# Performance work log

Hardware: AMD Instinct MI355X
Metric: run time of the kernel (lower is better)

Reference implementation:

```python
import jax, jax.numpy as jnp
import numpy as np

B, T, D, H = 2, 2048, 1024, 16
DH = D // H  # 64, rope dim


def rotate_half(x):
    x1, x2 = jnp.split(x, 2, axis=-1)
    return jnp.concatenate([-x2, x1], axis=-1)


def rope_tables(seq_len, dim, dtype=jnp.float32):
    inv_freq = 1.0 / (10000.0 ** (jnp.arange(0, dim, 2, dtype=jnp.float32) / dim))
    t = jnp.arange(seq_len, dtype=jnp.float32)
    freqs = jnp.outer(t, inv_freq)              # [T, dim/2]
    emb = jnp.concatenate([freqs, freqs], -1)   # [T, dim]
    return jnp.cos(emb).astype(dtype), jnp.sin(emb).astype(dtype)


def setup_inputs() -> dict:
    key = jax.random.key(0)
    ks = jax.random.split(key, 5)
    w_scale = 0.02
    x = jax.random.normal(ks[0], (B, T, D), jnp.float32)
    W_q = jax.random.normal(ks[1], (D, D), jnp.float32) * w_scale
    W_k = jax.random.normal(ks[2], (D, D), jnp.float32) * w_scale
    W_v = jax.random.normal(ks[3], (D, D), jnp.float32) * w_scale
    W_o = jax.random.normal(ks[4], (D, D), jnp.float32) * w_scale
    mask = jnp.tril(jnp.ones((T, T), jnp.int32))  # causal
    return {"x": x, "W_q": W_q, "W_k": W_k, "W_v": W_v, "W_o": W_o, "mask": mask}


def reference(x, W_q, W_k, W_v, W_o, mask):
    b, t, d = x.shape
    # Linear (bias=False): y = x @ W^T, weight shape (out, in)
    def proj(W):
        y = jnp.einsum('btd,ed->bte', x, W)
        return y.reshape(b, t, H, DH).transpose(0, 2, 1, 3)  # [B,H,T,dh]
    q, k, v = proj(W_q), proj(W_k), proj(W_v)

    cos, sin = rope_tables(t, DH, x.dtype)
    cos = cos[None, None]  # [1,1,T,dh]
    sin = sin[None, None]
    q = q * cos + rotate_half(q) * sin
    k = k * cos + rotate_half(k) * sin

    scale = 1.0 / np.sqrt(DH).astype(np.float32)
    scores = jnp.einsum('bhqd,bhkd->bhqk', q, k) * scale  # [B,H,T,T]
    neg_inf = jnp.finfo(scores.dtype).min
    scores = jnp.where(mask[:t, :t][None, None] == 0, neg_inf, scores)
    attn = jax.nn.softmax(scores, axis=-1)
    out = jnp.einsum('bhqk,bhkd->bhqd', attn, v)
    out = out.transpose(0, 2, 1, 3).reshape(b, t, d)
    return jnp.einsum('btd,ed->bte', out, W_o)
```

## Files before the change

kernel.cpp:

```cpp
#include <hip/hip_runtime.h>
#include <hip/hip_bf16.h>
#include <math.h>

#define B_  2
#define T_  2048
#define D_  1024
#define H_  16
#define DH_ 64
#define WN_ (D_ * D_)

typedef __attribute__((ext_vector_type(8))) short bf16x8;
typedef __attribute__((ext_vector_type(4))) float f32x4;

__device__ __forceinline__ void gll16(const void* g, void* l) {
  __builtin_amdgcn_global_load_lds(
      (const __attribute__((address_space(1))) void*)g,
      (__attribute__((address_space(3))) void*)l, 16, 0, 0);
}

__device__ __forceinline__ void storeC(float* p, float v) { *p = v; }
__device__ __forceinline__ void storeC(__hip_bfloat16* p, float v) {
  *p = __float2bfloat16(v);
}

__global__ __launch_bounds__(256)
void cvt_f32_bf16(const float* __restrict__ in, __hip_bfloat16* __restrict__ out,
                  int n4) {
  const int i = blockIdx.x * 256 + threadIdx.x;
  if (i >= n4) return;
  const float4 a = ((const float4*)in)[i];
  __hip_bfloat16 h0 = __float2bfloat16(a.x);
  __hip_bfloat16 h1 = __float2bfloat16(a.y);
  __hip_bfloat16 h2 = __float2bfloat16(a.z);
  __hip_bfloat16 h3 = __float2bfloat16(a.w);
  ushort4 o;
  o.x = *(unsigned short*)&h0;
  o.y = *(unsigned short*)&h1;
  o.z = *(unsigned short*)&h2;
  o.w = *(unsigned short*)&h3;
  *(ushort4*)(out + (size_t)i * 4) = o;
}

__global__ __launch_bounds__(256)
void cvt3_w(const float* __restrict__ Wq, const float* __restrict__ Wk,
            const float* __restrict__ Wv, __hip_bfloat16* __restrict__ out) {
  const int i = blockIdx.x * 256 + threadIdx.x;
  const int per = WN_ / 4;
  const int sel = i >> 18;
  const int off = i & (per - 1);
  const float* src = sel == 0 ? Wq : (sel == 1 ? Wk : Wv);
  const float4 a = ((const float4*)src)[off];
  __hip_bfloat16 h0 = __float2bfloat16(a.x);
  __hip_bfloat16 h1 = __float2bfloat16(a.y);
  __hip_bfloat16 h2 = __float2bfloat16(a.z);
  __hip_bfloat16 h3 = __float2bfloat16(a.w);
  ushort4 o;
  o.x = *(unsigned short*)&h0;
  o.y = *(unsigned short*)&h1;
  o.z = *(unsigned short*)&h2;
  o.w = *(unsigned short*)&h3;
  *(ushort4*)(out + (size_t)sel * WN_ + (size_t)off * 4) = o;
}

template <typename CT>
__global__ __launch_bounds__(256)
void gemm_bf16_mfma(const __hip_bfloat16* __restrict__ A,
                    const __hip_bfloat16* __restrict__ W,
                    CT* __restrict__ C, int M, int N, int K) {
  __shared__ unsigned short As[128 * 32];
  __shared__ unsigned short Bs[128 * 32];
  const int tid = threadIdx.x;
  const int w = tid >> 6;
  const int lane = tid & 63;
  const int lg = lane >> 4;
  const int ln = lane & 15;
  const int wr = w >> 1, wc = w & 1;
  const int row0 = blockIdx.y * 128;
  const int col0 = blockIdx.x * 128;

  const int sr = w * 32 + (lane >> 2);
  const int sp = lane & 3;

  f32x4 acc[4][4];
#pragma unroll
  for (int m = 0; m < 4; ++m)
#pragma unroll
    for (int n = 0; n < 4; ++n) acc[m][n] = (f32x4){0.f, 0.f, 0.f, 0.f};

  for (int k0 = 0; k0 < K; k0 += 32) {
#pragma unroll
    for (int c = 0; c < 2; ++c) {
      const int r = sr + c * 16;
      const int ks = sp ^ ((r >> 1) & 3);
      gll16(A + (size_t)(row0 + r) * K + k0 + ks * 8,
            &As[(w * 32 + c * 16) * 32]);
      gll16(W + (size_t)(col0 + r) * K + k0 + ks * 8,
            &Bs[(w * 32 + c * 16) * 32]);
    }
    __syncthreads();

    bf16x8 af[4], bfr[4];
#pragma unroll
    for (int m = 0; m < 4; ++m) {
      const int r = wr * 64 + m * 16 + ln;
      af[m] = *(const bf16x8*)&As[r * 32 + (lg ^ ((r >> 1) & 3)) * 8];
    }
#pragma unroll
    for (int n = 0; n < 4; ++n) {
      const int r = wc * 64 + n * 16 + ln;
      bfr[n] = *(const bf16x8*)&Bs[r * 32 + (lg ^ ((r >> 1) & 3)) * 8];
    }
#pragma unroll
    for (int m = 0; m < 4; ++m)
#pragma unroll
      for (int n = 0; n < 4; ++n)
        acc[m][n] = __builtin_amdgcn_mfma_f32_16x16x32_bf16(af[m], bfr[n],
                                                            acc[m][n], 0, 0, 0);
    __syncthreads();
  }

#pragma unroll
  for (int m = 0; m < 4; ++m) {
#pragma unroll
    for (int reg = 0; reg < 4; ++reg) {
      CT* crow = C + (size_t)(row0 + wr * 64 + m * 16 + lg * 4 + reg) * N
                 + col0 + wc * 64;
#pragma unroll
      for (int n = 0; n < 4; ++n) storeC(&crow[n * 16 + ln], acc[m][n][reg]);
    }
  }
}

__global__ __launch_bounds__(256)
void rope_qkv(const __hip_bfloat16* __restrict__ qkv,
              __hip_bfloat16* __restrict__ Qb, __hip_bfloat16* __restrict__ Kb) {
  const int idx = blockIdx.x * 256 + threadIdx.x;
  const int i = idx & 31;
  const int rest = idx >> 5;
  const int row = rest >> 4;
  const int h = rest & 15;
  const int t = row & (T_ - 1);
  const float inv_freq = powf(10000.0f, -(float)i * (1.0f / 32.0f));
  const float ang = (float)t * inv_freq;
  const float c = cosf(ang), s = sinf(ang);
  const size_t rb = (size_t)row * 3072 + h * 64;
  const float q1 = __bfloat162float(qkv[rb + i]);
  const float q2 = __bfloat162float(qkv[rb + i + 32]);
  const float k1 = __bfloat162float(qkv[rb + 1024 + i]);
  const float k2 = __bfloat162float(qkv[rb + 1024 + i + 32]);
  const size_t base = (size_t)rest * DH_;
  Qb[base + i]      = __float2bfloat16((q1 * c - q2 * s) * 0.125f);
  Qb[base + i + 32] = __float2bfloat16((q2 * c + q1 * s) * 0.125f);
  Kb[base + i]      = __float2bfloat16(k1 * c - k2 * s);
  Kb[base + i + 32] = __float2bfloat16(k2 * c + k1 * s);
}

__global__ __launch_bounds__(256)
void vt_prep(const __hip_bfloat16* __restrict__ qkv,
             __hip_bfloat16* __restrict__ vt) {
  __shared__ unsigned short Ls[64][65];
  const int tt = blockIdx.x;
  const int bh = blockIdx.y;
  const int b = bh >> 4, h = bh & 15;
  const int tid = threadIdx.x;
  const int t0 = tt * 64;
  const int rb = tid >> 3, c0 = (tid & 7) * 8;
#pragma unroll
  for (int it = 0; it < 2; ++it) {
    const int r = it * 32 + rb;
    uint4 x = *(const uint4*)&qkv[(size_t)(b * T_ + t0 + r) * 3072 + 2048 +
                                  h * 64 + c0];
    const unsigned short* xs = (const unsigned short*)&x;
#pragma unroll
    for (int j = 0; j < 8; ++j) Ls[c0 + j][r] = xs[j];
  }
  __syncthreads();
  const int d = tid >> 2, t8 = (tid & 3) * 16;
  unsigned short tmp[16];
#pragma unroll
  for (int j = 0; j < 16; ++j) tmp[j] = Ls[d][t8 + j];
  __hip_bfloat16* dst = vt + ((size_t)(b * H_ + h) * 64 + d) * T_ + t0 + t8;
  *(uint4*)&dst[0] = *(uint4*)&tmp[0];
  *(uint4*)&dst[8] = *(uint4*)&tmp[8];
}

#define SWZ(row, col) ((col) ^ (((row) & 7) << 3))

__global__ __launch_bounds__(256)
void attn_mfma(const __hip_bfloat16* __restrict__ Qb,
               const __hip_bfloat16* __restrict__ Kb,
               const __hip_bfloat16* __restrict__ vt,
               __hip_bfloat16* __restrict__ O) {
  __shared__ unsigned short Qs[64 * 64];
  __shared__ unsigned short Ks[64 * 64];
  __shared__ unsigned short Vt[64 * 64];
  __shared__ unsigned short Ps[4 * 16 * 64];

  const int bx = blockIdx.x;
  const int bh = blockIdx.y;
  const int b = bh >> 4, h = bh & 15;
  const int tid = threadIdx.x;
  const int w = tid >> 6;
  const int lane = tid & 63;
  const int lg = lane >> 4;
  const int ln = lane & 15;

  const size_t headoff = (size_t)b * T_ * D_ + (size_t)h * DH_;
  const __hip_bfloat16* Qg = Qb + headoff;
  const __hip_bfloat16* Kg = Kb + headoff;
  const __hip_bfloat16* vtg = vt + (size_t)(b * H_ + h) * 64 * T_;
  __hip_bfloat16* Og = O + headoff;

  const int rb = tid >> 3, c0 = (tid & 7) * 8;

  for (int pass = 0; pass < 2; ++pass) {
    const int qt = pass ? bx : 31 - bx;

#pragma unroll
    for (int it = 0; it < 2; ++it) {
      const int r = it * 32 + rb;
      uint4 x = *(const uint4*)(Qg + (size_t)(qt * 64 + r) * D_ + c0);
      *(uint4*)&Qs[r * 64 + SWZ(r, c0)] = x;
    }

    uint4 kreg[2], vreg[2];
#pragma unroll
    for (int it = 0; it < 2; ++it) {
      const int r = it * 32 + rb;
      kreg[it] = *(const uint4*)(Kg + (size_t)r * D_ + c0);
      vreg[it] = *(const uint4*)(vtg + (size_t)r * T_ + c0);
    }

    float m_run[4], l_run[4];
    f32x4 accO[4];
#pragma unroll
    for (int r = 0; r < 4; ++r) {
      m_run[r] = -3.0e38f;
      l_run[r] = 0.f;
      accO[r] = (f32x4){0.f, 0.f, 0.f, 0.f};
    }
    bf16x8 aQ[2];

    for (int kt = 0; kt <= qt; ++kt) {
      __syncthreads();
#pragma unroll
      for (int it = 0; it < 2; ++it) {
        const int r = it * 32 + rb;
        *(uint4*)&Ks[r * 64 + SWZ(r, c0)] = kreg[it];
        *(uint4*)&Vt[r * 64 + SWZ(r, c0)] = vreg[it];
      }
      __syncthreads();

      if (kt == 0) {
#pragma unroll
        for (int ks = 0; ks < 2; ++ks) {
          const int r = w * 16 + ln;
          aQ[ks] = *(const bf16x8*)&Qs[r * 64 + SWZ(r, lg * 8 + 32 * ks)];
        }
      }
      if (kt < qt) {
#pragma unroll
        for (int it = 0; it < 2; ++it) {
          const int r = it * 32 + rb;
          kreg[it] = *(const uint4*)(Kg + (size_t)((kt + 1) * 64 + r) * D_ + c0);
          vreg[it] = *(const uint4*)(vtg + (size_t)r * T_ + (kt + 1) * 64 + c0);
        }
      }

      f32x4 sf[4];
#pragma unroll
      for (int cb = 0; cb < 4; ++cb) sf[cb] = (f32x4){0.f, 0.f, 0.f, 0.f};
#pragma unroll
      for (int ks = 0; ks < 2; ++ks) {
#pragma unroll
        for (int cb = 0; cb < 4; ++cb) {
          const int r = cb * 16 + ln;
          bf16x8 bk = *(const bf16x8*)&Ks[r * 64 + SWZ(r, lg * 8 + 32 * ks)];
          sf[cb] = __builtin_amdgcn_mfma_f32_16x16x32_bf16(aQ[ks], bk, sf[cb], 0, 0, 0);
        }
      }

      if (kt == qt) {
#pragma unroll
        for (int cb = 0; cb < 4; ++cb) {
          const int col = cb * 16 + ln;
#pragma unroll
          for (int reg = 0; reg < 4; ++reg) {
            const int row = w * 16 + lg * 4 + reg;
            if (col > row) sf[cb][reg] = -3.0e38f;
          }
        }
      }

#pragma unroll
      for (int reg = 0; reg < 4; ++reg) {
        float mloc = fmaxf(fmaxf(sf[0][reg], sf[1][reg]),
                           fmaxf(sf[2][reg], sf[3][reg]));
        mloc = fmaxf(mloc, __shfl_xor(mloc, 1, 16));
        mloc = fmaxf(mloc, __shfl_xor(mloc, 2, 16));
        mloc = fmaxf(mloc, __shfl_xor(mloc, 4, 16));
        mloc = fmaxf(mloc, __shfl_xor(mloc, 8, 16));
        const float mnew = fmaxf(m_run[reg], mloc);
        const float alpha = __expf(m_run[reg] - mnew);
        m_run[reg] = mnew;
        float rsum = 0.f;
#pragma unroll
        for (int cb = 0; cb < 4; ++cb) {
          const float p = __expf(sf[cb][reg] - mnew);
          sf[cb][reg] = p;
          rsum += p;
        }
        rsum += __shfl_xor(rsum, 1, 16);
        rsum += __shfl_xor(rsum, 2, 16);
        rsum += __shfl_xor(rsum, 4, 16);
        rsum += __shfl_xor(rsum, 8, 16);
        l_run[reg] = l_run[reg] * alpha + rsum;
#pragma unroll
        for (int db = 0; db < 4; ++db) accO[db][reg] *= alpha;
      }

#pragma unroll
      for (int cb = 0; cb < 4; ++cb) {
        const int col = cb * 16 + ln;
#pragma unroll
        for (int reg = 0; reg < 4; ++reg) {
          const int row = lg * 4 + reg;
          *(__hip_bfloat16*)&Ps[w * 1024 + row * 64 + SWZ(row, col)] =
              __float2bfloat16(sf[cb][reg]);
        }
      }

#pragma unroll
      for (int ks = 0; ks < 2; ++ks) {
        bf16x8 ap =
            *(const bf16x8*)&Ps[w * 1024 + ln * 64 + SWZ(ln, lg * 8 + 32 * ks)];
#pragma unroll
        for (int db = 0; db < 4; ++db) {
          const int r = db * 16 + ln;
          bf16x8 bv = *(const bf16x8*)&Vt[r * 64 + SWZ(r, lg * 8 + 32 * ks)];
          accO[db] = __builtin_amdgcn_mfma_f32_16x16x32_bf16(ap, bv, accO[db], 0, 0, 0);
        }
      }
    }

#pragma unroll
    for (int reg = 0; reg < 4; ++reg) {
      const float inv = 1.0f / l_run[reg];
      const int qrow = qt * 64 + w * 16 + lg * 4 + reg;
#pragma unroll
      for (int db = 0; db < 4; ++db) {
        Og[(size_t)qrow * D_ + db * 16 + ln] =
            __float2bfloat16(accO[db][reg] * inv);
      }
    }
  }
}

extern "C" void kernel_launch(void* const* d_in, const int* in_sizes, int n_in,
                              void* d_out, int out_size, void* d_ws, size_t ws_size,
                              hipStream_t stream) {
  const float* x  = (const float*)d_in[0];
  const float* Wq = (const float*)d_in[1];
  const float* Wk = (const float*)d_in[2];
  const float* Wv = (const float*)d_in[3];
  const float* Wo = (const float*)d_in[4];
  float* out = (float*)d_out;

  const size_t NE = (size_t)B_ * T_ * D_;
  char* base = (char*)d_ws;
  __hip_bfloat16* qkvb  = (__hip_bfloat16*)base;
  __hip_bfloat16* xb    = (__hip_bfloat16*)(base + 3 * NE * 2);
  __hip_bfloat16* Wqkvb = (__hip_bfloat16*)(base + 4 * NE * 2);
  __hip_bfloat16* qb    = (__hip_bfloat16*)(base + 4 * NE * 2 + 3ull * WN_ * 2);
  __hip_bfloat16* kb    = qb + NE;
  __hip_bfloat16* vtb   = kb + NE;
  __hip_bfloat16* aob   = qkvb;
  __hip_bfloat16* Wob   = Wqkvb;

  cvt_f32_bf16<<<(int)(NE / 4 / 256), 256, 0, stream>>>(x, xb, (int)(NE / 4));
  cvt3_w<<<3 * WN_ / 4 / 256, 256, 0, stream>>>(Wq, Wk, Wv, Wqkvb);

  const dim3 gq(3 * D_ / 128, (B_ * T_) / 128);
  gemm_bf16_mfma<__hip_bfloat16><<<gq, 256, 0, stream>>>(
      xb, Wqkvb, qkvb, B_ * T_, 3 * D_, D_);

  rope_qkv<<<(B_ * T_ * H_ * 32) / 256, 256, 0, stream>>>(qkvb, qb, kb);
  vt_prep<<<dim3(T_ / 64, B_ * H_), 256, 0, stream>>>(qkvb, vtb);

  const dim3 ga(T_ / 128, B_ * H_);
  attn_mfma<<<ga, 256, 0, stream>>>(qb, kb, vtb, aob);

  cvt_f32_bf16<<<WN_ / 4 / 256, 256, 0, stream>>>(Wo, Wob, WN_ / 4);

  const dim3 go(D_ / 128, (B_ * T_) / 128);
  gemm_bf16_mfma<float><<<go, 256, 0, stream>>>(aob, Wob, out, B_ * T_, D_, D_);
}
```

Baseline: 274.7 us.

## Rewrite attention with 32x32 MFMA, transposed scores, and double-buffered K/V

```diff
diff --git a/kernel.cpp b/kernel.cpp
--- a/kernel.cpp
+++ b/kernel.cpp
@@ -11,6 +11,7 @@
 
 typedef __attribute__((ext_vector_type(8))) short bf16x8;
 typedef __attribute__((ext_vector_type(4))) float f32x4;
+typedef __attribute__((ext_vector_type(16))) float f32x16;
 
 __device__ __forceinline__ void gll16(const void* g, void* l) {
   __builtin_amdgcn_global_load_lds(
@@ -186,15 +187,14 @@
 
 #define SWZ(row, col) ((col) ^ (((row) & 7) << 3))
 
-__global__ __launch_bounds__(256)
-void attn_mfma(const __hip_bfloat16* __restrict__ Qb,
-               const __hip_bfloat16* __restrict__ Kb,
-               const __hip_bfloat16* __restrict__ vt,
-               __hip_bfloat16* __restrict__ O) {
-  __shared__ unsigned short Qs[64 * 64];
-  __shared__ unsigned short Ks[64 * 64];
-  __shared__ unsigned short Vt[64 * 64];
-  __shared__ unsigned short Ps[4 * 16 * 64];
+__global__ __launch_bounds__(128)
+void attn_mfma32(const __hip_bfloat16* __restrict__ Qb,
+                 const __hip_bfloat16* __restrict__ Kb,
+                 const __hip_bfloat16* __restrict__ vt,
+                 __hip_bfloat16* __restrict__ O) {
+  __shared__ unsigned short Ks[2][64 * 64];
+  __shared__ unsigned short Vs[2][64 * 64];
+  __shared__ unsigned short Ps[2][32 * 64];
 
   const int bx = blockIdx.x;
   const int bh = blockIdx.y;
@@ -202,8 +202,8 @@
   const int tid = threadIdx.x;
   const int w = tid >> 6;
   const int lane = tid & 63;
-  const int lg = lane >> 4;
-  const int ln = lane & 15;
+  const int lq = lane & 31;
+  const int hi = lane >> 5;
 
   const size_t headoff = (size_t)b * T_ * D_ + (size_t)h * DH_;
   const __hip_bfloat16* Qg = Qb + headoff;
@@ -211,146 +211,158 @@
   const __hip_bfloat16* vtg = vt + (size_t)(b * H_ + h) * 64 * T_;
   __hip_bfloat16* Og = O + headoff;
 
-  const int rb = tid >> 3, c0 = (tid & 7) * 8;
+  const int sr0 = tid >> 3;
+  const int sc0 = (tid & 7) * 8;
 
   for (int pass = 0; pass < 2; ++pass) {
     const int qt = pass ? bx : 31 - bx;
-
-#pragma unroll
-    for (int it = 0; it < 2; ++it) {
-      const int r = it * 32 + rb;
-      uint4 x = *(const uint4*)(Qg + (size_t)(qt * 64 + r) * D_ + c0);
-      *(uint4*)&Qs[r * 64 + SWZ(r, c0)] = x;
-    }
-
-    uint4 kreg[2], vreg[2];
-#pragma unroll
-    for (int it = 0; it < 2; ++it) {
-      const int r = it * 32 + rb;
-      kreg[it] = *(const uint4*)(Kg + (size_t)r * D_ + c0);
-      vreg[it] = *(const uint4*)(vtg + (size_t)r * T_ + c0);
-    }
-
-    float m_run[4], l_run[4];
-    f32x4 accO[4];
-#pragma unroll
-    for (int r = 0; r < 4; ++r) {
-      m_run[r] = -3.0e38f;
-      l_run[r] = 0.f;
-      accO[r] = (f32x4){0.f, 0.f, 0.f, 0.f};
-    }
-    bf16x8 aQ[2];
+    const int q_glob = qt * 64 + w * 32 + lq;
+
+    bf16x8 qf[4];
+#pragma unroll
+    for (int ks = 0; ks < 4; ++ks)
+      qf[ks] = *(const bf16x8*)(Qg + (size_t)q_glob * D_ + ks * 16 + hi * 8);
+
+    uint4 kreg[4], vreg[4];
+#pragma unroll
+    for (int it = 0; it < 4; ++it) {
+      const int r = sr0 + it * 16;
+      kreg[it] = *(const uint4*)(Kg + (size_t)r * D_ + sc0);
+      vreg[it] = *(const uint4*)(vtg + (size_t)r * T_ + sc0);
+    }
+#pragma unroll
+    for (int it = 0; it < 4; ++it) {
+      const int r = sr0 + it * 16;
+      *(uint4*)&Ks[0][r * 64 + SWZ(r, sc0)] = kreg[it];
+      *(uint4*)&Vs[0][r * 64 + SWZ(r, sc0)] = vreg[it];
+    }
+    if (qt >= 1) {
+#pragma unroll
+      for (int it = 0; it < 4; ++it) {
+        const int r = sr0 + it * 16;
+        kreg[it] = *(const uint4*)(Kg + (size_t)(64 + r) * D_ + sc0);
+        vreg[it] = *(const uint4*)(vtg + (size_t)r * T_ + 64 + sc0);
+      }
+    }
+
+    float m_run = -3.0e38f, l_run = 0.f;
+    f32x16 accO[2];
+#pragma unroll
+    for (int reg = 0; reg < 16; ++reg) { accO[0][reg] = 0.f; accO[1][reg] = 0.f; }
+
+    __syncthreads();
 
     for (int kt = 0; kt <= qt; ++kt) {
+      const int buf = kt & 1;
+      if (kt + 1 <= qt) {
+#pragma unroll
+        for (int it = 0; it < 4; ++it) {
+          const int r = sr0 + it * 16;
+          *(uint4*)&Ks[buf ^ 1][r * 64 + SWZ(r, sc0)] = kreg[it];
+          *(uint4*)&Vs[buf ^ 1][r * 64 + SWZ(r, sc0)] = vreg[it];
+        }
+      }
+      if (kt + 2 <= qt) {
+#pragma unroll
+        for (int it = 0; it < 4; ++it) {
+          const int r = sr0 + it * 16;
+          kreg[it] = *(const uint4*)(Kg + (size_t)((kt + 2) * 64 + r) * D_ + sc0);
+          vreg[it] = *(const uint4*)(vtg + (size_t)r * T_ + (kt + 2) * 64 + sc0);
+        }
+      }
+
+      f32x16 sf[2];
+#pragma unroll
+      for (int reg = 0; reg < 16; ++reg) { sf[0][reg] = 0.f; sf[1][reg] = 0.f; }
+#pragma unroll
+      for (int ks = 0; ks < 4; ++ks) {
+        const int c = ks * 16 + hi * 8;
+        bf16x8 ka0 = *(const bf16x8*)&Ks[buf][lq * 64 + SWZ(lq, c)];
+        bf16x8 ka1 = *(const bf16x8*)&Ks[buf][(32 + lq) * 64 + SWZ(32 + lq, c)];
+        sf[0] = __builtin_amdgcn_mfma_f32_32x32x16_bf16(ka0, qf[ks], sf[0], 0, 0, 0);
+        sf[1] = __builtin_amdgcn_mfma_f32_32x32x16_bf16(ka1, qf[ks], sf[1], 0, 0, 0);
+      }
+
+      const int kv0 = kt * 64;
+      if (kt == qt) {
+#pragma unroll
+        for (int reg = 0; reg < 16; ++reg) {
+          const int krow = (reg & 3) + 8 * (reg >> 2) + 4 * hi;
+          if (kv0 + krow > q_glob)      sf[0][reg] = -3.0e38f;
+          if (kv0 + 32 + krow > q_glob) sf[1][reg] = -3.0e38f;
+        }
+      }
+
+      float pmax = -3.0e38f;
+#pragma unroll
+      for (int reg = 0; reg < 16; ++reg)
+        pmax = fmaxf(pmax, fmaxf(sf[0][reg], sf[1][reg]));
+      pmax = fmaxf(pmax, __shfl_xor(pmax, 32, 64));
+      const float mnew = fmaxf(m_run, pmax);
+      const float alpha = __expf(m_run - mnew);
+      m_run = mnew;
+      float rsum = 0.f;
+#pragma unroll
+      for (int reg = 0; reg < 16; ++reg) {
+        sf[0][reg] = __expf(sf[0][reg] - mnew);
+        sf[1][reg] = __expf(sf[1][reg] - mnew);
+        rsum += sf[0][reg] + sf[1][reg];
+      }
+      rsum += __shfl_xor(rsum, 32, 64);
+      l_run = l_run * alpha + rsum;
+#pragma unroll
+      for (int reg = 0; reg < 16; ++reg) {
+        accO[0][reg] *= alpha;
+        accO[1][reg] *= alpha;
+      }
+
+#pragma unroll
+      for (int kb = 0; kb < 2; ++kb) {
+#pragma unroll
+        for (int j = 0; j < 4; ++j) {
+          __hip_bfloat16 b0 = __float2bfloat16(sf[kb][4 * j + 0]);
+          __hip_bfloat16 b1 = __float2bfloat16(sf[kb][4 * j + 1]);
+          __hip_bfloat16 b2 = __float2bfloat16(sf[kb][4 * j + 2]);
+          __hip_bfloat16 b3 = __float2bfloat16(sf[kb][4 * j + 3]);
+          uint2 pk;
+          pk.x = (unsigned)*(unsigned short*)&b0 |
+                 ((unsigned)*(unsigned short*)&b1 << 16);
+          pk.y = (unsigned)*(unsigned short*)&b2 |
+                 ((unsigned)*(unsigned short*)&b3 << 16);
+          const int col = kb * 32 + 8 * j + 4 * hi;
+          *(uint2*)&Ps[w][lq * 64 + SWZ(lq, col)] = pk;
+        }
+      }
+
+#pragma unroll
+      for (int ks = 0; ks < 4; ++ks) {
+        const int c = ks * 16 + hi * 8;
+        bf16x8 pb  = *(const bf16x8*)&Ps[w][lq * 64 + SWZ(lq, c)];
+        bf16x8 va0 = *(const bf16x8*)&Vs[buf][lq * 64 + SWZ(lq, c)];
+        bf16x8 va1 = *(const bf16x8*)&Vs[buf][(32 + lq) * 64 + SWZ(32 + lq, c)];
+        accO[0] = __builtin_amdgcn_mfma_f32_32x32x16_bf16(va0, pb, accO[0], 0, 0, 0);
+        accO[1] = __builtin_amdgcn_mfma_f32_32x32x16_bf16(va1, pb, accO[1], 0, 0, 0);
+      }
+
       __syncthreads();
-#pragma unroll
-      for (int it = 0; it < 2; ++it) {
-        const int r = it * 32 + rb;
-        *(uint4*)&Ks[r * 64 + SWZ(r, c0)] = kreg[it];
-        *(uint4*)&Vt[r * 64 + SWZ(r, c0)] = vreg[it];
-      }
-      __syncthreads();
-
-      if (kt == 0) {
-#pragma unroll
-        for (int ks = 0; ks < 2; ++ks) {
-          const int r = w * 16 + ln;
-          aQ[ks] = *(const bf16x8*)&Qs[r * 64 + SWZ(r, lg * 8 + 32 * ks)];
-        }
-      }
-      if (kt < qt) {
-#pragma unroll
-        for (int it = 0; it < 2; ++it) {
-          const int r = it * 32 + rb;
-          kreg[it] = *(const uint4*)(Kg + (size_t)((kt + 1) * 64 + r) * D_ + c0);
-          vreg[it] = *(const uint4*)(vtg + (size_t)r * T_ + (kt + 1) * 64 + c0);
-        }
-      }
-
-      f32x4 sf[4];
-#pragma unroll
-      for (int cb = 0; cb < 4; ++cb) sf[cb] = (f32x4){0.f, 0.f, 0.f, 0.f};
-#pragma unroll
-      for (int ks = 0; ks < 2; ++ks) {
-#pragma unroll
-        for (int cb = 0; cb < 4; ++cb) {
-          const int r = cb * 16 + ln;
-          bf16x8 bk = *(const bf16x8*)&Ks[r * 64 + SWZ(r, lg * 8 + 32 * ks)];
-          sf[cb] = __builtin_amdgcn_mfma_f32_16x16x32_bf16(aQ[ks], bk, sf[cb], 0, 0, 0);
-        }
-      }
-
-      if (kt == qt) {
-#pragma unroll
-        for (int cb = 0; cb < 4; ++cb) {
-          const int col = cb * 16 + ln;
-#pragma unroll
-          for (int reg = 0; reg < 4; ++reg) {
-            const int row = w * 16 + lg * 4 + reg;
-            if (col > row) sf[cb][reg] = -3.0e38f;
-          }
-        }
-      }
-
-#pragma unroll
-      for (int reg = 0; reg < 4; ++reg) {
-        float mloc = fmaxf(fmaxf(sf[0][reg], sf[1][reg]),
-                           fmaxf(sf[2][reg], sf[3][reg]));
-        mloc = fmaxf(mloc, __shfl_xor(mloc, 1, 16));
-        mloc = fmaxf(mloc, __shfl_xor(mloc, 2, 16));
-        mloc = fmaxf(mloc, __shfl_xor(mloc, 4, 16));
-        mloc = fmaxf(mloc, __shfl_xor(mloc, 8, 16));
-        const float mnew = fmaxf(m_run[reg], mloc);
-        const float alpha = __expf(m_run[reg] - mnew);
-        m_run[reg] = mnew;
-        float rsum = 0.f;
-#pragma unroll
-        for (int cb = 0; cb < 4; ++cb) {
-          const float p = __expf(sf[cb][reg] - mnew);
-          sf[cb][reg] = p;
-          rsum += p;
-        }
-        rsum += __shfl_xor(rsum, 1, 16);
-        rsum += __shfl_xor(rsum, 2, 16);
-        rsum += __shfl_xor(rsum, 4, 16);
-        rsum += __shfl_xor(rsum, 8, 16);
-        l_run[reg] = l_run[reg] * alpha + rsum;
-#pragma unroll
-        for (int db = 0; db < 4; ++db) accO[db][reg] *= alpha;
-      }
-
-#pragma unroll
-      for (int cb = 0; cb < 4; ++cb) {
-        const int col = cb * 16 + ln;
-#pragma unroll
-        for (int reg = 0; reg < 4; ++reg) {
-          const int row = lg * 4 + reg;
-          *(__hip_bfloat16*)&Ps[w * 1024 + row * 64 + SWZ(row, col)] =
-              __float2bfloat16(sf[cb][reg]);
-        }
-      }
-
-#pragma unroll
-      for (int ks = 0; ks < 2; ++ks) {
-        bf16x8 ap =
-            *(const bf16x8*)&Ps[w * 1024 + ln * 64 + SWZ(ln, lg * 8 + 32 * ks)];
-#pragma unroll
-        for (int db = 0; db < 4; ++db) {
-          const int r = db * 16 + ln;
-          bf16x8 bv = *(const bf16x8*)&Vt[r * 64 + SWZ(r, lg * 8 + 32 * ks)];
-          accO[db] = __builtin_amdgcn_mfma_f32_16x16x32_bf16(ap, bv, accO[db], 0, 0, 0);
-        }
-      }
-    }
-
-#pragma unroll
-    for (int reg = 0; reg < 4; ++reg) {
-      const float inv = 1.0f / l_run[reg];
-      const int qrow = qt * 64 + w * 16 + lg * 4 + reg;
-#pragma unroll
-      for (int db = 0; db < 4; ++db) {
-        Og[(size_t)qrow * D_ + db * 16 + ln] =
-            __float2bfloat16(accO[db][reg] * inv);
+    }
+
+    const float inv = 1.0f / l_run;
+#pragma unroll
+    for (int db = 0; db < 2; ++db) {
+#pragma unroll
+      for (int j = 0; j < 4; ++j) {
+        __hip_bfloat16 b0 = __float2bfloat16(accO[db][4 * j + 0] * inv);
+        __hip_bfloat16 b1 = __float2bfloat16(accO[db][4 * j + 1] * inv);
+        __hip_bfloat16 b2 = __float2bfloat16(accO[db][4 * j + 2] * inv);
+        __hip_bfloat16 b3 = __float2bfloat16(accO[db][4 * j + 3] * inv);
+        uint2 pk;
+        pk.x = (unsigned)*(unsigned short*)&b0 |
+               ((unsigned)*(unsigned short*)&b1 << 16);
+        pk.y = (unsigned)*(unsigned short*)&b2 |
+               ((unsigned)*(unsigned short*)&b3 << 16);
+        const int d = db * 32 + 8 * j + 4 * hi;
+        *(uint2*)(Og + (size_t)q_glob * D_ + d) = pk;
       }
     }
   }
@@ -388,7 +400,7 @@
   vt_prep<<<dim3(T_ / 64, B_ * H_), 256, 0, stream>>>(qkvb, vtb);
 
   const dim3 ga(T_ / 128, B_ * H_);
-  attn_mfma<<<ga, 256, 0, stream>>>(qb, kb, vtb, aob);
+  attn_mfma32<<<ga, 128, 0, stream>>>(qb, kb, vtb, aob);
 
   cvt_f32_bf16<<<WN_ / 4 / 256, 256, 0, stream>>>(Wo, Wob, WN_ / 4);
 
```

Measured after the change: 276.7 us. No clear change (+0.7%).
